# Optimization experiments

Hardware: AMD Instinct MI355X
Metric: run time of the kernel (lower is better)

## Reference

```python
import jax, jax.numpy as jnp
import numpy as np

B, T, D = 2, 4096, 1024
H, DK, DV = 8, 128, 128   # head dims (expand_k = expand_v = 1.0)
INTER = 4096
CHUNK = 128
EPS = 1e-5


def rmsnorm(x, w, eps=EPS):
    return x * jax.lax.rsqrt(jnp.mean(x * x, axis=-1, keepdims=True) + eps) * w


def linear_attention(x, Wq, Wk, Wv, Wo, out_norm_w):
    # identity feature map, causal linear attention, per-head RMSNorm output norm
    b, t, d = x.shape
    n = t // CHUNK
    q = (x @ Wq).reshape(b, t, H, DK).transpose(0, 2, 1, 3)  # [B,H,T,DK]
    k = (x @ Wk).reshape(b, t, H, DK).transpose(0, 2, 1, 3)
    v = (x @ Wv).reshape(b, t, H, DV).transpose(0, 2, 1, 3)
    # chunked O(T * d^2) causal linear attention
    qc = q.reshape(b, H, n, CHUNK, DK).transpose(2, 0, 1, 3, 4)  # [N,B,H,C,DK]
    kc = k.reshape(b, H, n, CHUNK, DK).transpose(2, 0, 1, 3, 4)
    vc = v.reshape(b, H, n, CHUNK, DV).transpose(2, 0, 1, 3, 4)
    causal = jnp.tril(jnp.ones((CHUNK, CHUNK), dtype=bool))

    def step(S, qkv):
        qb, kb, vb = qkv  # each [B,H,C,d]
        attn = jnp.einsum('bhid,bhjd->bhij', qb, kb)
        attn = jnp.where(causal, attn, 0.0)
        o = jnp.einsum('bhij,bhjv->bhiv', attn, vb) + jnp.einsum('bhid,bhdv->bhiv', qb, S)
        S = S + jnp.einsum('bhid,bhiv->bhdv', kb, vb)
        return S, o

    S0 = jnp.zeros((b, H, DK, DV), x.dtype)
    _, o = jax.lax.scan(step, S0, (qc, kc, vc))      # o: [N,B,H,C,DV]
    o = o.transpose(1, 2, 0, 3, 4).reshape(b, H, t, DV)
    o = rmsnorm(o, out_norm_w)                        # per-head output RMSNorm
    o = o.transpose(0, 2, 1, 3).reshape(b, t, H * DV)
    return o @ Wo


def setup_inputs() -> dict:
    key = jax.random.key(0)
    ks = jax.random.split(key, 9)
    s = 0.02
    return {
        'hidden_states': jax.random.normal(ks[0], (B, T, D), jnp.float32),
        'attn_norm_w': jnp.ones((D,), jnp.float32),
        'Wq': jax.random.normal(ks[1], (D, H * DK), jnp.float32) * s,
        'Wk': jax.random.normal(ks[2], (D, H * DK), jnp.float32) * s,
        'Wv': jax.random.normal(ks[3], (D, H * DV), jnp.float32) * s,
        'Wo': jax.random.normal(ks[4], (H * DV, D), jnp.float32) * s,
        'attn_out_norm_w': jnp.ones((DV,), jnp.float32),
        'mlp_norm_w': jnp.ones((D,), jnp.float32),
        'Wgate': jax.random.normal(ks[5], (D, INTER), jnp.float32) * s,
        'Wup': jax.random.normal(ks[6], (D, INTER), jnp.float32) * s,
        'Wdown': jax.random.normal(ks[7], (INTER, D), jnp.float32) * s,
    }


def reference(hidden_states, attn_norm_w, Wq, Wk, Wv, Wo, attn_out_norm_w,
              mlp_norm_w, Wgate, Wup, Wdown):
    x = hidden_states
    # attn sub-block: RMSNorm -> linear attention -> residual
    h = rmsnorm(x, attn_norm_w)
    x = x + linear_attention(h, Wq, Wk, Wv, Wo, attn_out_norm_w)
    # mlp sub-block: RMSNorm -> SwiGLU -> residual
    h = rmsnorm(x, mlp_norm_w)
    x = x + (jax.nn.silu(h @ Wgate) * (h @ Wup)) @ Wdown
    return x
```

## Files before the change

### kernel.cpp

```cpp
#include <hip/hip_runtime.h>
#include <hip/hip_bf16.h>
#include <stdint.h>


typedef __hip_bfloat16 bf16;
typedef __bf16 bf16x8 __attribute__((ext_vector_type(8)));
typedef float f32x4 __attribute__((ext_vector_type(4)));

union Frag {
  uint4 u;
  bf16x8 b;
  unsigned short s[8];
};

__device__ __forceinline__ float bf2f(unsigned short v) {
  union { unsigned int u; float f; } c;
  c.u = (unsigned int)v << 16;
  return c.f;
}
__device__ __forceinline__ unsigned short f2bf(float f) {
  union { float f; unsigned int u; } c;
  c.f = f;
  unsigned int u = c.u;
  u += 0x7fffu + ((u >> 16) & 1u);
  return (unsigned short)(u >> 16);
}

__device__ __forceinline__ void gload16(const unsigned short* g, unsigned short* l) {
  __builtin_amdgcn_global_load_lds(
      (const __attribute__((address_space(1))) unsigned int*)g,
      (__attribute__((address_space(3))) unsigned int*)l, 16, 0, 0);
}

__global__ __launch_bounds__(256) void k_rmsnorm(const float* __restrict__ x,
                                                 const float* __restrict__ w,
                                                 bf16* __restrict__ out) {
  const int row = blockIdx.x;
  const int t = threadIdx.x;
  float4 v = reinterpret_cast<const float4*>(x + (size_t)row * 1024)[t];
  float ss = v.x * v.x + v.y * v.y + v.z * v.z + v.w * v.w;
#pragma unroll
  for (int o = 32; o > 0; o >>= 1) ss += __shfl_xor(ss, o, 64);
  __shared__ float red[4];
  if ((t & 63) == 0) red[t >> 6] = ss;
  __syncthreads();
  float tot = red[0] + red[1] + red[2] + red[3];
  float sc = rsqrtf(tot * (1.f / 1024.f) + 1e-5f);
  float4 wv = reinterpret_cast<const float4*>(w)[t];
  ushort4 o4;
  o4.x = f2bf(v.x * sc * wv.x);
  o4.y = f2bf(v.y * sc * wv.y);
  o4.z = f2bf(v.z * sc * wv.z);
  o4.w = f2bf(v.w * sc * wv.w);
  reinterpret_cast<ushort4*>(out + (size_t)row * 1024)[t] = o4;
}

struct TP4 {
  const float* s[4];
  bf16* d[4];
};
__global__ __launch_bounds__(256) void k_transpose_w4(TP4 p) {
  __shared__ float tile[32][33];
  const int z = blockIdx.z;
  const float* W = p.s[z];
  unsigned short* WTu = (unsigned short*)p.d[z];
  const int bx = blockIdx.x * 32;
  const int by = blockIdx.y * 32;
  const int tx = threadIdx.x, ty = threadIdx.y;
#pragma unroll
  for (int i = 0; i < 4; i++)
    tile[ty + i * 8][tx] = W[(size_t)(by + ty + i * 8) * 1024 + bx + tx];
  __syncthreads();
#pragma unroll
  for (int i = 0; i < 4; i++)
    WTu[(size_t)(bx + ty + i * 8) * 1024 + by + tx] = f2bf(tile[tx][ty + i * 8]);
}

__global__ __launch_bounds__(256) void k_transpose_w(const float* __restrict__ W,
                                                     bf16* __restrict__ WT,
                                                     int R, int C) {
  __shared__ float tile[32][33];
  const int bx = blockIdx.x * 32;
  const int by = blockIdx.y * 32;
  const int tx = threadIdx.x, ty = threadIdx.y;
#pragma unroll
  for (int i = 0; i < 4; i++)
    tile[ty + i * 8][tx] = W[(size_t)(by + ty + i * 8) * C + bx + tx];
  __syncthreads();
  unsigned short* WTu = (unsigned short*)WT;
#pragma unroll
  for (int i = 0; i < 4; i++)
    WTu[(size_t)(bx + ty + i * 8) * R + by + tx] = f2bf(tile[tx][ty + i * 8]);
}

__global__ __launch_bounds__(256) void k_transpose_wgu(const float* __restrict__ Wg,
                                                       const float* __restrict__ Wu,
                                                       bf16* __restrict__ WT) {
  __shared__ float tile[32][33];
  const int which = blockIdx.z;
  const float* W = which ? Wu : Wg;
  const int bx = blockIdx.x * 32;
  const int by = blockIdx.y * 32;
  const int tx = threadIdx.x, ty = threadIdx.y;
#pragma unroll
  for (int i = 0; i < 4; i++)
    tile[ty + i * 8][tx] = W[(size_t)(by + ty + i * 8) * 4096 + bx + tx];
  __syncthreads();
  unsigned short* WTu = (unsigned short*)WT;
#pragma unroll
  for (int i = 0; i < 4; i++) {
    const int c = bx + ty + i * 8;
    const int fr = ((c >> 6) << 7) + which * 64 + (c & 63);
    WTu[(size_t)fr * 1024 + by + tx] = f2bf(tile[tx][ty + i * 8]);
  }
}

template <int EPI>
__global__ __launch_bounds__(256, 2) void k_gemm128(const bf16* __restrict__ A, int lda,
                                                    const bf16* __restrict__ BT,
                                                    const float* __restrict__ res,
                                                    void* __restrict__ Cout,
                                                    int N, int K) {
  constexpr int SLOTSZ = 16384;
  __shared__ __align__(16) unsigned short lds[2 * SLOTSZ];

  const int gx = gridDim.x;
  const int nwg = gx * gridDim.y;
  const int lin = blockIdx.y * gx + blockIdx.x;
  const int swz = (lin & 7) * (nwg >> 3) + (lin >> 3);
  const int bm = (swz / gx) * 128, bn = (swz % gx) * 128;

  const int t = threadIdx.x;
  const int wid = t >> 6, lane = t & 63;
  const int wr = wid >> 1, wc = wid & 1;
  const int lm = lane & 15, kg = lane >> 4;
  const int x0 = ((kg ^ (lm & 7)) << 3);
  const int x1 = (((4 + kg) ^ (lm & 7)) << 3);
  const int srow = t >> 3;
  const int scolS = (((t & 7) ^ (srow & 7)) << 3);

  const unsigned short* Ab = (const unsigned short*)A;
  const unsigned short* Bb = (const unsigned short*)BT;

  auto stage = [&](int s, int tt) {
#pragma unroll
    for (int g = 0; g < 4; g++)
      gload16(Ab + (size_t)(bm + g * 32 + srow) * lda + (size_t)tt * 64 + scolS,
              &lds[s * SLOTSZ + g * 2048 + wid * 512]);
#pragma unroll
    for (int g = 0; g < 4; g++)
      gload16(Bb + (size_t)(bn + g * 32 + srow) * K + (size_t)tt * 64 + scolS,
              &lds[s * SLOTSZ + 8192 + g * 2048 + wid * 512]);
  };

  f32x4 acc[4][4] = {};
  Frag af[4][2], bf[4][2];

  const int NT = K / 64;
  stage(0, 0);
  stage(1, 1);
  asm volatile("s_waitcnt vmcnt(8)" ::: "memory");
  __builtin_amdgcn_s_barrier();

  for (int i = 0; i < NT; i++) {
    const int s = i & 1;
    const int ab = s * SLOTSZ;
#pragma unroll
    for (int m = 0; m < 4; m++) {
      const int r = (wr * 64 + m * 16 + lm) * 64;
      af[m][0].u = *(const uint4*)&lds[ab + r + x0];
      af[m][1].u = *(const uint4*)&lds[ab + r + x1];
    }
#pragma unroll
    for (int n = 0; n < 4; n++) {
      const int r = 8192 + (wc * 64 + n * 16 + lm) * 64;
      bf[n][0].u = *(const uint4*)&lds[ab + r + x0];
      bf[n][1].u = *(const uint4*)&lds[ab + r + x1];
    }
    asm volatile("s_waitcnt lgkmcnt(0)" ::: "memory");
    __builtin_amdgcn_s_barrier();
    if (i + 2 < NT) {
      stage(s, i + 2);
      asm volatile("s_waitcnt vmcnt(8)" ::: "memory");
    } else {
      asm volatile("s_waitcnt vmcnt(0)" ::: "memory");
    }
    __builtin_amdgcn_s_barrier();
    __builtin_amdgcn_s_setprio(1);
#pragma unroll
    for (int m = 0; m < 4; m++)
#pragma unroll
      for (int n = 0; n < 4; n++) {
        acc[m][n] = __builtin_amdgcn_mfma_f32_16x16x32_bf16(af[m][0].b, bf[n][0].b,
                                                            acc[m][n], 0, 0, 0);
        acc[m][n] = __builtin_amdgcn_mfma_f32_16x16x32_bf16(af[m][1].b, bf[n][1].b,
                                                            acc[m][n], 0, 0, 0);
      }
    __builtin_amdgcn_s_setprio(0);
  }

  if constexpr (EPI == 1) {
    float* fl = (float*)lds;
    float* Co = (float*)Cout;
#pragma unroll
    for (int p = 0; p < 2; p++) {
      __syncthreads();
      if (wr == p) {
#pragma unroll
        for (int m = 0; m < 4; m++)
#pragma unroll
          for (int n = 0; n < 4; n++)
#pragma unroll
            for (int r = 0; r < 4; r++)
              fl[(m * 16 + kg * 4 + r) * 128 + wc * 64 + n * 16 + lm] = acc[m][n][r];
      }
      __syncthreads();
#pragma unroll
      for (int j = 0; j < 8; j++) {
        const int idx = t + j * 256;
        const int row = idx >> 5, c4 = (idx & 31) << 2;
        const size_t o = (size_t)(bm + p * 64 + row) * N + bn + c4;
        float4 v = *(const float4*)&fl[row * 128 + c4];
        float4 rv = *(const float4*)&res[o];
        v.x += rv.x; v.y += rv.y; v.z += rv.z; v.w += rv.w;
        *(float4*)&Co[o] = v;
      }
    }
  } else {
    __syncthreads();
#pragma unroll
    for (int m = 0; m < 4; m++)
#pragma unroll
      for (int n = 0; n < 4; n++)
#pragma unroll
        for (int r = 0; r < 4; r++)
          lds[(wr * 64 + m * 16 + kg * 4 + r) * 128 + wc * 64 + n * 16 + lm] =
              f2bf(acc[m][n][r]);
    __syncthreads();
    unsigned short* Cu = (unsigned short*)Cout;
    if constexpr (EPI == 0) {
#pragma unroll
      for (int j = 0; j < 8; j++) {
        const int idx = t + j * 256;
        const int row = idx >> 4, seg = idx & 15;
        *(uint4*)(Cu + (size_t)(bm + row) * N + bn + seg * 8) =
            *(const uint4*)&lds[row * 128 + seg * 8];
      }
    } else {
      const int No = N >> 1;
#pragma unroll
      for (int j = 0; j < 4; j++) {
        const int idx = t + j * 256;
        const int row = idx >> 3, s8 = (idx & 7) << 3;
        Frag gf, uf, rr;
        gf.u = *(const uint4*)&lds[row * 128 + s8];
        uf.u = *(const uint4*)&lds[row * 128 + 64 + s8];
#pragma unroll
        for (int a = 0; a < 8; a++) {
          float g = bf2f(gf.s[a]);
          float uu = bf2f(uf.s[a]);
          rr.s[a] = f2bf(g / (1.f + __expf(-g)) * uu);
        }
        *(uint4*)(Cu + (size_t)(bm + row) * No + (bn >> 1) + s8) = rr.u;
      }
    }
  }
}

__global__ __launch_bounds__(256) void k_chunk_kv(const bf16* __restrict__ qkv,
                                                  float* __restrict__ G,
                                                  bf16* __restrict__ VT) {
  __shared__ __align__(16) unsigned short ks[128][128];
  __shared__ __align__(16) unsigned short vs[128][136];
  const int idx = blockIdx.x;
  const int cc = idx & 31, bh = idx >> 5, bb = bh >> 3, hh = bh & 7;
  const unsigned short* qkvu = (const unsigned short*)qkv;
  const unsigned short* kp = qkvu + (size_t)(bb * 4096 + cc * 128) * 3072 + 1024 + hh * 128;
  const unsigned short* vp = kp + 1024;
  const int t = threadIdx.x;
#pragma unroll
  for (int i = 0; i < 8; i++) {
    int ch = t + i * 256;
    int r = ch >> 4, c8 = (ch & 15) << 3;
    *(uint4*)&ks[r][c8] = *(const uint4*)(kp + (size_t)r * 3072 + c8);
    *(uint4*)&vs[r][c8] = *(const uint4*)(vp + (size_t)r * 3072 + c8);
  }
  __syncthreads();
  const int dv0 = (t >> 4) * 8, dk0 = (t & 15) * 8;
  float acc[8][8] = {};
  for (int j = 0; j < 128; j++) {
    Frag kf, vf;
    vf.u = *(const uint4*)&vs[j][dv0];
    kf.u = *(const uint4*)&ks[j][dk0];
    float kx[8], vx[8];
#pragma unroll
    for (int a = 0; a < 8; a++) { kx[a] = bf2f(kf.s[a]); vx[a] = bf2f(vf.s[a]); }
#pragma unroll
    for (int a = 0; a < 8; a++)
#pragma unroll
      for (int b2 = 0; b2 < 8; b2++) acc[a][b2] += vx[a] * kx[b2];
  }
  float* Gp = G + (size_t)idx * 16384;
#pragma unroll
  for (int a = 0; a < 8; a++)
#pragma unroll
    for (int b2 = 0; b2 < 8; b2 += 4) {
      float4 w4 = make_float4(acc[a][b2], acc[a][b2 + 1], acc[a][b2 + 2], acc[a][b2 + 3]);
      *(float4*)(Gp + (size_t)(dv0 + a) * 128 + dk0 + b2) = w4;
    }
  unsigned short* vo = (unsigned short*)VT + (size_t)bh * 524288 + cc * 128;
#pragma unroll
  for (int i = 0; i < 8; i++) {
    const int dv = (t >> 4) + i * 16;
    const int r0 = (t & 15) * 8;
    Frag f;
#pragma unroll
    for (int j = 0; j < 8; j++) f.s[j] = vs[r0 + j][dv];
    *(uint4*)(vo + (size_t)dv * 4096 + r0) = f.u;
  }
}

__global__ __launch_bounds__(256) void k_prefix(const float* __restrict__ G,
                                                bf16* __restrict__ S) {
  const size_t gid = (size_t)blockIdx.x * 256 + threadIdx.x;
  const size_t bh = gid >> 14, e = gid & 16383;
  const float* gp = G + (bh << 5) * 16384 + e;
  unsigned short* sp = (unsigned short*)S + (bh << 5) * 16384 + e;
  float run = 0.f;
  for (int c2 = 0; c2 < 32; c2++) {
    sp[(size_t)c2 << 14] = f2bf(run);
    run += gp[(size_t)c2 << 14];
  }
}

__global__ __launch_bounds__(256) void k_attn2(const bf16* __restrict__ qkv,
                                               const bf16* __restrict__ VT,
                                               const bf16* __restrict__ ST,
                                               const float* __restrict__ nw,
                                               bf16* __restrict__ A2) {
  __shared__ __align__(16) unsigned short Qs[128][136];
  __shared__ __align__(16) unsigned short Ks[128][136];
  __shared__ __align__(16) unsigned short Bs[128][136];
  __shared__ float red[128][2];

  const int idx = blockIdx.x;
  const int cc = idx & 31, bh = idx >> 5, bb = bh >> 3, hh = bh & 7;
  const size_t rowbase = (size_t)(bb * 4096 + cc * 128);
  const unsigned short* qp = (const unsigned short*)qkv + rowbase * 3072 + hh * 128;
  const unsigned short* kp = qp + 1024;
  const unsigned short* vtp = (const unsigned short*)VT + (size_t)bh * 524288 + cc * 128;
  const unsigned short* stp = (const unsigned short*)ST + ((size_t)idx << 14);

  const int t = threadIdx.x;
  const int wid = t >> 6, lane = t & 63;
  const int wm = (wid >> 1) * 64, wn = (wid & 1) * 64;
  const int lm = lane & 15, kg = lane >> 4;
  const int sr = t >> 4;
  const int sc = (t & 15) << 3;

#pragma unroll
  for (int i = 0; i < 8; i++) {
    int r = sr + i * 16;
    *(uint4*)&Qs[r][sc] = *(const uint4*)(qp + (size_t)r * 3072 + sc);
    *(uint4*)&Ks[r][sc] = *(const uint4*)(kp + (size_t)r * 3072 + sc);
    *(uint4*)&Bs[r][sc] = *(const uint4*)(vtp + (size_t)r * 4096 + sc);
  }
  __syncthreads();

  f32x4 acc[4][4] = {};
#pragma unroll
  for (int kk = 0; kk < 4; kk++) {
    Frag af[4], bfr[4];
#pragma unroll
    for (int i = 0; i < 4; i++) {
      af[i].u = *(const uint4*)&Qs[wm + i * 16 + lm][kk * 32 + kg * 8];
      bfr[i].u = *(const uint4*)&Ks[wn + i * 16 + lm][kk * 32 + kg * 8];
    }
#pragma unroll
    for (int mi = 0; mi < 4; mi++)
#pragma unroll
      for (int ni = 0; ni < 4; ni++)
        acc[mi][ni] = __builtin_amdgcn_mfma_f32_16x16x32_bf16(af[mi].b, bfr[ni].b,
                                                              acc[mi][ni], 0, 0, 0);
  }
  __syncthreads();

#pragma unroll
  for (int mi = 0; mi < 4; mi++)
#pragma unroll
    for (int r = 0; r < 4; r++) {
      const int gi = wm + mi * 16 + kg * 4 + r;
#pragma unroll
      for (int ni = 0; ni < 4; ni++) {
        const int gj = wn + ni * 16 + lm;
        Ks[gi][gj] = f2bf(gj <= gi ? acc[mi][ni][r] : 0.f);
      }
    }
  __syncthreads();

  f32x4 oa[4][4] = {};
#pragma unroll
  for (int kk = 0; kk < 4; kk++) {
    Frag af[4], bfr[4];
#pragma unroll
    for (int i = 0; i < 4; i++) {
      af[i].u = *(const uint4*)&Ks[wm + i * 16 + lm][kk * 32 + kg * 8];
      bfr[i].u = *(const uint4*)&Bs[wn + i * 16 + lm][kk * 32 + kg * 8];
    }
#pragma unroll
    for (int mi = 0; mi < 4; mi++)
#pragma unroll
      for (int ni = 0; ni < 4; ni++)
        oa[mi][ni] = __builtin_amdgcn_mfma_f32_16x16x32_bf16(af[mi].b, bfr[ni].b,
                                                             oa[mi][ni], 0, 0, 0);
  }
  __syncthreads();

#pragma unroll
  for (int i = 0; i < 8; i++) {
    int r = sr + i * 16;
    *(uint4*)&Bs[r][sc] = *(const uint4*)(stp + (size_t)r * 128 + sc);
  }
  __syncthreads();

#pragma unroll
  for (int kk = 0; kk < 4; kk++) {
    Frag af[4], bfr[4];
#pragma unroll
    for (int i = 0; i < 4; i++) {
      af[i].u = *(const uint4*)&Qs[wm + i * 16 + lm][kk * 32 + kg * 8];
      bfr[i].u = *(const uint4*)&Bs[wn + i * 16 + lm][kk * 32 + kg * 8];
    }
#pragma unroll
    for (int mi = 0; mi < 4; mi++)
#pragma unroll
      for (int ni = 0; ni < 4; ni++)
        oa[mi][ni] = __builtin_amdgcn_mfma_f32_16x16x32_bf16(af[mi].b, bfr[ni].b,
                                                             oa[mi][ni], 0, 0, 0);
  }

#pragma unroll
  for (int mi = 0; mi < 4; mi++)
#pragma unroll
    for (int r = 0; r < 4; r++) {
      float ss = 0.f;
#pragma unroll
      for (int ni = 0; ni < 4; ni++) ss += oa[mi][ni][r] * oa[mi][ni][r];
      ss += __shfl_xor(ss, 1, 64);
      ss += __shfl_xor(ss, 2, 64);
      ss += __shfl_xor(ss, 4, 64);
      ss += __shfl_xor(ss, 8, 64);
      if (lm == 0) red[wm + mi * 16 + kg * 4 + r][wid & 1] = ss;
    }
  __syncthreads();

#pragma unroll
  for (int mi = 0; mi < 4; mi++)
#pragma unroll
    for (int r = 0; r < 4; r++) {
      const int gi = wm + mi * 16 + kg * 4 + r;
      const float tot = red[gi][0] + red[gi][1];
      const float scl = rsqrtf(tot * (1.f / 128.f) + 1e-5f);
#pragma unroll
      for (int ni = 0; ni < 4; ni++) {
        const int gj = wn + ni * 16 + lm;
        Ks[gi][gj] = f2bf(oa[mi][ni][r] * scl * nw[gj]);
      }
    }
  __syncthreads();

  unsigned short* A2u = (unsigned short*)A2;
#pragma unroll
  for (int i = 0; i < 8; i++) {
    int r = sr + i * 16;
    *(uint4*)(A2u + (rowbase + r) * 1024 + hh * 128 + sc) = *(const uint4*)&Ks[r][sc];
  }
}

extern "C" void kernel_launch(void* const* d_in, const int* in_sizes, int n_in,
                              void* d_out, int out_size, void* d_ws, size_t ws_size,
                              hipStream_t stream) {
  const float* x = (const float*)d_in[0];
  const float* anw = (const float*)d_in[1];
  const float* Wq = (const float*)d_in[2];
  const float* Wk = (const float*)d_in[3];
  const float* Wv = (const float*)d_in[4];
  const float* Wo = (const float*)d_in[5];
  const float* onw = (const float*)d_in[6];
  const float* mnw = (const float*)d_in[7];
  const float* Wg = (const float*)d_in[8];
  const float* Wu = (const float*)d_in[9];
  const float* Wd = (const float*)d_in[10];
  float* out = (float*)d_out;

  char* base = (char*)d_ws;
  size_t off = 0;
  auto alloc = [&](size_t bytes) -> char* {
    char* q = base + off;
    off += (bytes + 255) & ~(size_t)255;
    return q;
  };
  bf16* WqkvT = (bf16*)alloc(3072ll * 1024 * 2);
  bf16* WoT   = (bf16*)alloc(1024ll * 1024 * 2);
  bf16* WguT  = (bf16*)alloc(8192ll * 1024 * 2);
  bf16* WdT   = (bf16*)alloc(1024ll * 4096 * 2);
  bf16* h     = (bf16*)alloc(8192ll * 1024 * 2);
  float* x1   = (float*)alloc(8192ll * 1024 * 4);
  char* pool  = alloc(8192ll * 3072 * 2 + 16ll * 32 * 16384 * 4 +
                      16ll * 32 * 16384 * 2 + 16ll * 128 * 4096 * 2);
  bf16* qkv = (bf16*)pool;
  float* G  = (float*)(pool + 8192ll * 3072 * 2);
  bf16* S   = (bf16*)(pool + 8192ll * 3072 * 2 + 16ll * 32 * 16384 * 4);
  bf16* VT  = (bf16*)(pool + 8192ll * 3072 * 2 + 16ll * 32 * 16384 * 4 +
                      16ll * 32 * 16384 * 2);
  bf16* act = (bf16*)pool;

  const dim3 tb32(32, 8);
  TP4 tp;
  tp.s[0] = Wq; tp.d[0] = WqkvT;
  tp.s[1] = Wk; tp.d[1] = WqkvT + 1024ll * 1024;
  tp.s[2] = Wv; tp.d[2] = WqkvT + 2048ll * 1024;
  tp.s[3] = Wo; tp.d[3] = WoT;
  k_transpose_w4<<<dim3(32, 32, 4), tb32, 0, stream>>>(tp);
  k_transpose_wgu<<<dim3(128, 32, 2), tb32, 0, stream>>>(Wg, Wu, WguT);
  k_transpose_w<<<dim3(32, 128), tb32, 0, stream>>>(Wd, WdT, 4096, 1024);

  k_rmsnorm<<<8192, 256, 0, stream>>>(x, anw, h);
  k_gemm128<0><<<dim3(24, 64), 256, 0, stream>>>(h, 1024, WqkvT, nullptr, qkv, 3072, 1024);
  k_chunk_kv<<<512, 256, 0, stream>>>(qkv, G, VT);
  k_prefix<<<1024, 256, 0, stream>>>(G, S);
  k_attn2<<<512, 256, 0, stream>>>(qkv, VT, S, onw, h);
  k_gemm128<1><<<dim3(8, 64), 256, 0, stream>>>(h, 1024, WoT, x, x1, 1024, 1024);

  k_rmsnorm<<<8192, 256, 0, stream>>>(x1, mnw, h);
  k_gemm128<3><<<dim3(64, 64), 256, 0, stream>>>(h, 1024, WguT, nullptr, act, 8192, 1024);
  k_gemm128<1><<<dim3(8, 64), 256, 0, stream>>>(act, 4096, WdT, x1, out, 1024, 4096);
}
```

Baseline: 464.7 us.

## Add dedicated 128x256 gate/up GEMM kernel with 512 threads and SwiGLU epilogue

Replaces the generic 128x128 GEMM used for the fused gate/up projection with a specialized kernel that computes a 128x256 tile using 8 waves (512 threads). The weight interleave changes from 64-column to 128-column groups so each tile holds 128 gate and 128 up columns. This reuses each A tile across twice as many output columns and halves the number of workgroups. The SwiGLU epilogue moves into the new kernel, and the old EPI==3 path is removed. The cost is a larger per-block working set, and occupancy depends on how many registers each thread needs.

```diff
diff --git a/kernel.cpp b/kernel.cpp
--- a/kernel.cpp
+++ b/kernel.cpp
@@ -110,8 +110,107 @@
 #pragma unroll
   for (int i = 0; i < 4; i++) {
     const int c = bx + ty + i * 8;
-    const int fr = ((c >> 6) << 7) + which * 64 + (c & 63);
+    const int fr = ((c >> 7) << 8) + which * 128 + (c & 127);
     WTu[(size_t)fr * 1024 + by + tx] = f2bf(tile[tx][ty + i * 8]);
+  }
+}
+
+__global__ __launch_bounds__(512, 4) void k_gemm_gu(const bf16* __restrict__ A,
+                                                    const bf16* __restrict__ BT,
+                                                    bf16* __restrict__ Cout,
+                                                    int N, int K) {
+  constexpr int SLOTSZ = 12288;
+  __shared__ __align__(16) unsigned short lds[32768];
+
+  const int gx = gridDim.x;
+  const int nwg = gx * gridDim.y;
+  const int lin = blockIdx.y * gx + blockIdx.x;
+  const int swz = (lin & 7) * (nwg >> 3) + (lin >> 3);
+  const int bm = (swz / gx) * 128, bn = (swz % gx) * 256;
+
+  const int t = threadIdx.x;
+  const int wid = t >> 6, lane = t & 63;
+  const int wr = wid >> 2, wc = wid & 3;
+  const int lm = lane & 15, kg = lane >> 4;
+  const int xr = ((kg ^ (lm & 3) ^ (lm >> 2)) << 3);
+  const int scolS = (((t & 3) ^ ((t >> 2) & 3) ^ ((t >> 4) & 3)) << 3);
+  const int srow = t >> 2;
+
+  const unsigned short* Ab = (const unsigned short*)A;
+  const unsigned short* Bb = (const unsigned short*)BT;
+
+  auto stage = [&](int s, int tt) {
+    gload16(Ab + (size_t)(bm + srow) * 1024 + (size_t)tt * 32 + scolS,
+            &lds[s * SLOTSZ + t * 8]);
+#pragma unroll
+    for (int g = 0; g < 2; g++)
+      gload16(Bb + (size_t)(bn + g * 128 + srow) * K + (size_t)tt * 32 + scolS,
+              &lds[s * SLOTSZ + 4096 + g * 4096 + t * 8]);
+  };
+
+  f32x4 acc[4][4] = {};
+  Frag af[4], bf[4];
+
+  const int NT = K / 32;
+  stage(0, 0);
+  stage(1, 1);
+  asm volatile("s_waitcnt vmcnt(3)" ::: "memory");
+  __builtin_amdgcn_s_barrier();
+
+  for (int i = 0; i < NT; i++) {
+    const int s = i & 1;
+    const int ab = s * SLOTSZ;
+#pragma unroll
+    for (int m = 0; m < 4; m++)
+      af[m].u = *(const uint4*)&lds[ab + (wr * 64 + m * 16 + lm) * 32 + xr];
+#pragma unroll
+    for (int n = 0; n < 4; n++)
+      bf[n].u = *(const uint4*)&lds[ab + 4096 + (wc * 64 + n * 16 + lm) * 32 + xr];
+    asm volatile("s_waitcnt lgkmcnt(0)" ::: "memory");
+    __builtin_amdgcn_s_barrier();
+    if (i + 2 < NT) {
+      stage(s, i + 2);
+      asm volatile("s_waitcnt vmcnt(3)" ::: "memory");
+    } else {
+      asm volatile("s_waitcnt vmcnt(0)" ::: "memory");
+    }
+    __builtin_amdgcn_s_barrier();
+    __builtin_amdgcn_s_setprio(1);
+#pragma unroll
+    for (int m = 0; m < 4; m++)
+#pragma unroll
+      for (int n = 0; n < 4; n++)
+        acc[m][n] = __builtin_amdgcn_mfma_f32_16x16x32_bf16(af[m].b, bf[n].b,
+                                                            acc[m][n], 0, 0, 0);
+    __builtin_amdgcn_s_setprio(0);
+  }
+
+  __syncthreads();
+#pragma unroll
+  for (int m = 0; m < 4; m++)
+#pragma unroll
+    for (int n = 0; n < 4; n++)
+#pragma unroll
+      for (int r = 0; r < 4; r++)
+        lds[(wr * 64 + m * 16 + kg * 4 + r) * 256 + wc * 64 + n * 16 + lm] =
+            f2bf(acc[m][n][r]);
+  __syncthreads();
+  unsigned short* Cu = (unsigned short*)Cout;
+  const int No = N >> 1;
+#pragma unroll
+  for (int j = 0; j < 4; j++) {
+    const int idx = t + j * 512;
+    const int row = idx >> 4, seg = idx & 15;
+    Frag gf, uf, rr;
+    gf.u = *(const uint4*)&lds[row * 256 + seg * 8];
+    uf.u = *(const uint4*)&lds[row * 256 + 128 + seg * 8];
+#pragma unroll
+    for (int a = 0; a < 8; a++) {
+      float g = bf2f(gf.s[a]);
+      float uu = bf2f(uf.s[a]);
+      rr.s[a] = f2bf(g / (1.f + __expf(-g)) * uu);
+    }
+    *(uint4*)(Cu + (size_t)(bm + row) * No + (bn >> 1) + seg * 8) = rr.u;
   }
 }
 
@@ -238,31 +337,12 @@
               f2bf(acc[m][n][r]);
     __syncthreads();
     unsigned short* Cu = (unsigned short*)Cout;
-    if constexpr (EPI == 0) {
-#pragma unroll
-      for (int j = 0; j < 8; j++) {
-        const int idx = t + j * 256;
-        const int row = idx >> 4, seg = idx & 15;
-        *(uint4*)(Cu + (size_t)(bm + row) * N + bn + seg * 8) =
-            *(const uint4*)&lds[row * 128 + seg * 8];
-      }
-    } else {
-      const int No = N >> 1;
-#pragma unroll
-      for (int j = 0; j < 4; j++) {
-        const int idx = t + j * 256;
-        const int row = idx >> 3, s8 = (idx & 7) << 3;
-        Frag gf, uf, rr;
-        gf.u = *(const uint4*)&lds[row * 128 + s8];
-        uf.u = *(const uint4*)&lds[row * 128 + 64 + s8];
-#pragma unroll
-        for (int a = 0; a < 8; a++) {
-          float g = bf2f(gf.s[a]);
-          float uu = bf2f(uf.s[a]);
-          rr.s[a] = f2bf(g / (1.f + __expf(-g)) * uu);
-        }
-        *(uint4*)(Cu + (size_t)(bm + row) * No + (bn >> 1) + s8) = rr.u;
-      }
+#pragma unroll
+    for (int j = 0; j < 8; j++) {
+      const int idx = t + j * 256;
+      const int row = idx >> 4, seg = idx & 15;
+      *(uint4*)(Cu + (size_t)(bm + row) * N + bn + seg * 8) =
+          *(const uint4*)&lds[row * 128 + seg * 8];
     }
   }
 }
@@ -533,6 +613,6 @@
   k_gemm128<1><<<dim3(8, 64), 256, 0, stream>>>(h, 1024, WoT, x, x1, 1024, 1024);
 
   k_rmsnorm<<<8192, 256, 0, stream>>>(x1, mnw, h);
-  k_gemm128<3><<<dim3(64, 64), 256, 0, stream>>>(h, 1024, WguT, nullptr, act, 8192, 1024);
+  k_gemm_gu<<<dim3(32, 64), 512, 0, stream>>>(h, WguT, act, 8192, 1024);
   k_gemm128<1><<<dim3(8, 64), 256, 0, stream>>>(act, 4096, WdT, x1, out, 1024, 4096);
 }
```

Measured after the change: 441.7 us. 4.9% less time.
